# Kernel optimization log

Hardware: AMD Instinct MI355X
Metric: run time of the kernel (lower is better)

Reference implementation:

```python
import jax, jax.numpy as jnp
import numpy as np

HID, BOT, C, HEADS, K, SCALES, HZN = 32, 8, 16, 4, 3, 4, 12


def layer_norm(x, g, b, eps=1e-5):
    m = jnp.mean(x, axis=-1, keepdims=True)
    v = jnp.var(x, axis=-1, keepdims=True)
    return (x - m) * jax.lax.rsqrt(v + eps) * g + b


def setup_inputs() -> dict:
    B, T, N = 8, 32, 1500
    keys = iter(jax.random.split(jax.random.key(0), 64))
    def nrm(shape, s=0.05):
        return jax.random.normal(next(keys), shape, jnp.float32) * s
    x = jax.random.normal(next(keys), (B, T, N), jnp.float32)
    adj = (jax.random.uniform(next(keys), (N, N)) < 0.01).astype(jnp.float32)
    return dict(
        x=x, adj=adj,
        dw_w=nrm((1, 1, K)), dw_b=jnp.zeros((1,)),
        bn1_g=jnp.ones((1,)), bn1_b=jnp.zeros((1,)),
        pw_w=nrm((C, 1)), pw_b=jnp.zeros((C,)),
        bn2_g=jnp.ones((C,)), bn2_b=jnp.zeros((C,)),
        feat_w=nrm((C, HID)), feat_b=jnp.zeros((HID,)),
        scale_w=nrm((SCALES, HID, HID)), scale_b=jnp.zeros((SCALES, HID)),
        scale_ln_g=jnp.ones((SCALES, HID)), scale_ln_b=jnp.zeros((SCALES, HID)),
        fusion_weight=jnp.exp(-0.5 * jnp.arange(SCALES, dtype=jnp.float32)),
        fus_lo_w=nrm((HID, BOT)), fus_lo_b=jnp.zeros((BOT,)),
        fus_hi_w=nrm((BOT, HID)), fus_hi_b=jnp.zeros((HID,)),
        sp_ln_g=jnp.ones((HID,)), sp_ln_b=jnp.zeros((HID,)),
        qkv_lo_w=nrm((HID, 3 * BOT)), qkv_lo_b=jnp.zeros((3 * BOT,)),
        qkv_hi_w=nrm((3 * BOT, 3 * HID)), qkv_hi_b=jnp.zeros((3 * HID,)),
        graph_U=nrm((N, BOT)), graph_V=nrm((BOT, N)),
        adj_mix=jnp.array(0.0, jnp.float32), adj_scale=jnp.array(1.0, jnp.float32),
        out_lo_w=nrm((HID, BOT)), out_lo_b=jnp.zeros((BOT,)),
        out_hi_w=nrm((BOT, HID)), out_hi_b=jnp.zeros((HID,)),
        at_ln_g=jnp.ones((HID,)), at_ln_b=jnp.zeros((HID,)),
        pred_lo_w=nrm((HID, BOT)), pred_lo_b=jnp.zeros((BOT,)),
        mid_ln_g=jnp.ones((BOT,)), mid_ln_b=jnp.zeros((BOT,)),
        pred_hi_w=nrm((BOT, HZN)), pred_hi_b=jnp.zeros((HZN,)),
        log_decay=jnp.array(-2.3, jnp.float32),
        gate_w1=nrm((HID, BOT)), gate_b1=jnp.zeros((BOT,)),
        gate_w2=nrm((BOT, HZN)), gate_b2=jnp.zeros((HZN,)),
    )


def reference(x, adj, dw_w, dw_b, bn1_g, bn1_b, pw_w, pw_b, bn2_g, bn2_b,
              feat_w, feat_b, scale_w, scale_b, scale_ln_g, scale_ln_b,
              fusion_weight, fus_lo_w, fus_lo_b, fus_hi_w, fus_hi_b,
              sp_ln_g, sp_ln_b, qkv_lo_w, qkv_lo_b, qkv_hi_w, qkv_hi_b,
              graph_U, graph_V, adj_mix, adj_scale,
              out_lo_w, out_lo_b, out_hi_w, out_hi_b, at_ln_g, at_ln_b,
              pred_lo_w, pred_lo_b, mid_ln_g, mid_ln_b, pred_hi_w, pred_hi_b,
              log_decay, gate_w1, gate_b1, gate_w2, gate_b2):
    B, T, N = x.shape
    # ---- temporal feature extraction: depthwise-separable conv, eval-mode BN ----
    s = x.transpose(0, 2, 1).reshape(B * N, 1, T)  # per-node series [B*N,1,T]
    dw = jax.lax.conv_general_dilated(
        s, dw_w, (1,), 'SAME', dimension_numbers=('NCH', 'OIH', 'NCH'))
    dw = jax.nn.relu((dw + dw_b[None, :, None]) * bn1_g[None, :, None] + bn1_b[None, :, None])
    pw = jnp.einsum('bit,oi->bot', dw, pw_w) + pw_b[None, :, None]  # pointwise 1x1
    pw = jax.nn.relu(pw * bn2_g[None, :, None] + bn2_b[None, :, None])
    h = pw.mean(-1).reshape(B, N, C) @ feat_w + feat_b  # [B,N,HID]
    # ---- multi-scale spatial diffusion over adjacency powers ----
    eye = jnp.eye(N, dtype=x.dtype)
    a_hat = adj + eye
    a_hat = a_hat / (jnp.sum(a_hat, axis=-1, keepdims=True) + 1e-8)
    a2 = a_hat @ a_hat
    hops = [eye, a_hat, a2, a2 @ a_hat]
    feats = []
    for i in range(SCALES):  # fixed, small loop over scales
        agg = h if i == 0 else jnp.einsum('nm,bmh->bnh', hops[i], h)
        t = agg @ scale_w[i] + scale_b[i]
        feats.append(jax.nn.relu(layer_norm(t, scale_ln_g[i], scale_ln_b[i])))
    alpha = jax.nn.softmax(fusion_weight)
    fused = sum(alpha[i] * feats[i] for i in range(SCALES))
    out = (fused @ fus_lo_w + fus_lo_b) @ fus_hi_w + fus_hi_b  # bottleneck fusion
    h = layer_norm(out + h, sp_ln_g, sp_ln_b)
    # ---- low-rank adaptive graph attention ----
    qkv = (h @ qkv_lo_w + qkv_lo_b) @ qkv_hi_w + qkv_hi_b  # [B,N,3*HID]
    q, k, v = jnp.split(qkv, 3, axis=-1)
    hd = HID // HEADS
    to_heads = lambda t: t.reshape(B, N, HEADS, hd).transpose(0, 2, 1, 3)
    q, k, v = to_heads(q), to_heads(k), to_heads(v)
    scores = jnp.einsum('bhnd,bhmd->bhnm', q, k) / jnp.sqrt(jnp.float32(hd))
    struct = graph_U @ graph_V + jax.nn.sigmoid(adj_mix) * adj_scale * adj  # [N,N]
    attn = jax.nn.softmax(scores + struct[None, None], axis=-1)
    o = jnp.einsum('bhnm,bhmd->bhnd', attn, v).transpose(0, 2, 1, 3).reshape(B, N, HID)
    o = (o @ out_lo_w + out_lo_b) @ out_hi_w + out_hi_b
    h = layer_norm(o + h, at_ln_g, at_ln_b)
    # ---- gated horizon predictor with learned exponential decay ----
    x_mid = jax.nn.relu(layer_norm(h @ pred_lo_w + pred_lo_b, mid_ln_g, mid_ln_b))
    init_pred = x_mid @ pred_hi_w + pred_hi_b  # [B,N,HZN]
    gate = jax.nn.sigmoid(jax.nn.relu(h @ gate_w1 + gate_b1) @ gate_w2 + gate_b2)
    tdec = jnp.arange(1, HZN + 1, dtype=x.dtype)  # [HZN]
    prog = x[:, -1, :, None] * jnp.exp(-jnp.exp(log_decay) * tdec)
    return gate * init_pred + (1.0 - gate) * prog
```

## Files before the change

### kernel.cpp

```cpp
#include <hip/hip_runtime.h>
#include <math.h>

#define NN 1500
#define BB 8
#define TT 32
#define HIDD 32
#define BOTT 8
#define CC 16
#define NHEADS 4
#define NSCALES 4
#define HZNN 12
#define BC (BB*HIDD)
#define CAP 128
#define MC 128
#define PROWS 1536
#define KS_STRIDE 24
#define VS_STRIDE 136

typedef _Float16 f16;
typedef __attribute__((ext_vector_type(4))) _Float16 half4;
typedef __attribute__((ext_vector_type(4))) float floatx4;

__global__ void k_prep_temporal(const float* __restrict__ adj,
                                const float* __restrict__ gV,
                                int* __restrict__ sidx, float* __restrict__ sval,
                                float* __restrict__ sraw, int* __restrict__ scnt,
                                float* __restrict__ VgT,
                                f16* __restrict__ Qh, f16* __restrict__ Kh,
                                f16* __restrict__ VT,
                                const float* __restrict__ x,
    const float* __restrict__ dw_w, const float* __restrict__ dw_b,
    const float* __restrict__ bn1_g, const float* __restrict__ bn1_b,
    const float* __restrict__ pw_w, const float* __restrict__ pw_b,
    const float* __restrict__ bn2_g, const float* __restrict__ bn2_b,
    const float* __restrict__ feat_w, const float* __restrict__ feat_b,
    float* __restrict__ h0) {
  if (blockIdx.x < NN) {
    int n = blockIdx.x;
    int tid = threadIdx.x;
    const float* row = adj + (size_t)n * NN;
    __shared__ int cnt;
    __shared__ float red[4];
    __shared__ float s_inv;
    float ssum = 0.f;
    for (int m = tid; m < NN; m += 256) ssum += row[m];
    for (int off = 32; off > 0; off >>= 1) ssum += __shfl_down(ssum, off, 64);
    if ((tid & 63) == 0) red[tid >> 6] = ssum;
    if (tid == 0) cnt = 0;
    __syncthreads();
    if (tid == 0) {
      float tot = red[0] + red[1] + red[2] + red[3] + 1.0f;
      s_inv = 1.0f / (tot + 1e-8f);
    }
    __syncthreads();
    float inv = s_inv;
    for (int m = tid; m < NN; m += 256) {
      float a = row[m];
      if (a != 0.f || m == n) {
        int pos = atomicAdd(&cnt, 1);
        if (pos < CAP) {
          sidx[n * CAP + pos] = m;
          sval[n * CAP + pos] = (a + (m == n ? 1.f : 0.f)) * inv;
          sraw[n * CAP + pos] = a;
        }
      }
    }
    __syncthreads();
    if (tid == 0) scnt[n] = min(cnt, CAP);
    if (n == 0) {
      for (int m = tid; m < NN; m += 256) {
#pragma unroll
        for (int j = 0; j < 8; ++j) VgT[m * 8 + j] = gV[j * NN + m];
      }
    }
    if (n == 2) {
      for (int idx = tid; idx < 32 * 36 * 16; idx += 256) {
        int bb = idx / (36 * 16), rem = idx % (36 * 16);
        size_t off = ((size_t)bb * PROWS + NN + rem / 16) * 16 + (rem % 16);
        Qh[off] = (f16)0.f;
        Kh[off] = (f16)0.f;
      }
      for (int idx = tid; idx < 32 * PROWS; idx += 256) {
        int bb = idx / PROWS, m = idx % PROWS;
        VT[((size_t)bb * 16 + 8) * PROWS + m] = (f16)((m < NN) ? 1.f : 0.f);
      }
      for (int idx = tid; idx < 32 * 8 * 36; idx += 256) {
        int bb = idx / (8 * 36), rem = idx % (8 * 36);
        VT[((size_t)bb * 16 + rem / 36) * PROWS + NN + (rem % 36)] = (f16)0.f;
      }
    }
  } else {
    int tid = (blockIdx.x - NN) * 256 + threadIdx.x;
    if (tid >= BB * NN) return;
    int b = tid / NN, n = tid % NN;
    float s[TT];
#pragma unroll
    for (int t = 0; t < TT; ++t) s[t] = x[(size_t)b * TT * NN + (size_t)t * NN + n];
    float w0 = dw_w[0], w1 = dw_w[1], w2 = dw_w[2];
    float db = dw_b[0], g1v = bn1_g[0], b1v = bn1_b[0];
    float dwr[TT];
#pragma unroll
    for (int t = 0; t < TT; ++t) {
      float left  = (t > 0)      ? s[t - 1] : 0.f;
      float right = (t < TT - 1) ? s[t + 1] : 0.f;
      float v = left * w0 + s[t] * w1 + right * w2;
      v = (v + db) * g1v + b1v;
      dwr[t] = fmaxf(v, 0.f);
    }
    float mo[CC];
#pragma unroll
    for (int o = 0; o < CC; ++o) mo[o] = 0.f;
    for (int t = 0; t < TT; ++t) {
      float d = dwr[t];
#pragma unroll
      for (int o = 0; o < CC; ++o) {
        float v = (d * pw_w[o] + pw_b[o]) * bn2_g[o] + bn2_b[o];
        mo[o] += fmaxf(v, 0.f);
      }
    }
#pragma unroll
    for (int o = 0; o < CC; ++o) mo[o] *= (1.f / TT);
    float* dst = h0 + (size_t)n * BC + b * HIDD;
    for (int j = 0; j < HIDD; ++j) {
      float acc = feat_b[j];
#pragma unroll
      for (int o = 0; o < CC; ++o) acc += mo[o] * feat_w[o * HIDD + j];
      dst[j] = acc;
    }
  }
}

__global__ void k_spmm_sp(const int* __restrict__ sidx, const float* __restrict__ sval,
                          const int* __restrict__ scnt,
                          const float* __restrict__ X, float* __restrict__ Y) {
  int n = blockIdx.x;
  int tid = threadIdx.x;
  __shared__ int   li[CAP];
  __shared__ float lv[CAP];
  int cnt = scnt[n];
  if (tid < cnt) { li[tid] = sidx[n * CAP + tid]; lv[tid] = sval[n * CAP + tid]; }
  __syncthreads();
  float acc = 0.f;
  for (int e = 0; e < cnt; ++e) acc += lv[e] * X[(size_t)li[e] * BC + tid];
  Y[(size_t)n * BC + tid] = acc;
}

__global__ void k_fuse_qkv(
    const float* __restrict__ h0, const float* __restrict__ g1,
    const float* __restrict__ g2, const float* __restrict__ g3,
    const float* __restrict__ scale_w, const float* __restrict__ scale_b,
    const float* __restrict__ sln_g, const float* __restrict__ sln_b,
    const float* __restrict__ fusion_w,
    const float* __restrict__ fus_lo_w, const float* __restrict__ fus_lo_b,
    const float* __restrict__ fus_hi_w, const float* __restrict__ fus_hi_b,
    const float* __restrict__ sp_g, const float* __restrict__ sp_b,
    const float* __restrict__ qkv_lo_w, const float* __restrict__ qkv_lo_b,
    const float* __restrict__ qkv_hi_w, const float* __restrict__ qkv_hi_b,
    const float* __restrict__ gU, const float* __restrict__ VgT,
    float* __restrict__ h_out,
    float* __restrict__ Qw, float* __restrict__ Kw, float* __restrict__ Vw,
    f16* __restrict__ Qh, f16* __restrict__ Kh, f16* __restrict__ VT) {
  int tid = threadIdx.x;
  int gr = tid >> 4, l = tid & 15;
  int row = blockIdx.x * 16 + gr;
  int b = row / NN, n = row % NN;
  size_t rofs = (size_t)n * BC + b * HIDD;
  int j0 = 2 * l;
  float fw0 = fusion_w[0], fw1 = fusion_w[1], fw2 = fusion_w[2], fw3 = fusion_w[3];
  float fm = fmaxf(fmaxf(fw0, fw1), fmaxf(fw2, fw3));
  float e0 = __expf(fw0 - fm), e1 = __expf(fw1 - fm), e2 = __expf(fw2 - fm), e3 = __expf(fw3 - fm);
  float einv = 1.f / (e0 + e1 + e2 + e3);
  float alpha[4] = {e0 * einv, e1 * einv, e2 * einv, e3 * einv};
  const float* srcp[4] = {h0, g1, g2, g3};
  float fused[2] = {0.f, 0.f};
#pragma unroll
  for (int i = 0; i < NSCALES; ++i) {
    const float* sp = srcp[i] + rofs;
    float src[32];
#pragma unroll
    for (int k4 = 0; k4 < 8; ++k4) {
      float4 f = *(const float4*)(sp + k4 * 4);
      src[k4 * 4] = f.x; src[k4 * 4 + 1] = f.y; src[k4 * 4 + 2] = f.z; src[k4 * 4 + 3] = f.w;
    }
    const float* W = scale_w + i * HIDD * HIDD;
    float t0 = scale_b[i * HIDD + j0], t1v = scale_b[i * HIDD + j0 + 1];
#pragma unroll
    for (int k = 0; k < 32; ++k) {
      float2 w = *(const float2*)(W + k * HIDD + j0);
      t0 += src[k] * w.x; t1v += src[k] * w.y;
    }
    float s1 = t0 + t1v;
    float s2 = t0 * t0 + t1v * t1v;
    s1 += __shfl_xor(s1, 1, 16); s1 += __shfl_xor(s1, 2, 16);
    s1 += __shfl_xor(s1, 4, 16); s1 += __shfl_xor(s1, 8, 16);
    s2 += __shfl_xor(s2, 1, 16); s2 += __shfl_xor(s2, 2, 16);
    s2 += __shfl_xor(s2, 4, 16); s2 += __shfl_xor(s2, 8, 16);
    float mean = s1 * (1.f / 32.f);
    float var = s2 * (1.f / 32.f) - mean * mean;
    float r = rsqrtf(var + 1e-5f);
    float a = alpha[i];
    float tn0 = (t0 - mean) * r * sln_g[i * HIDD + j0] + sln_b[i * HIDD + j0];
    float tn1 = (t1v - mean) * r * sln_g[i * HIDD + j0 + 1] + sln_b[i * HIDD + j0 + 1];
    fused[0] += a * fmaxf(tn0, 0.f);
    fused[1] += a * fmaxf(tn1, 0.f);
  }
  float lo[BOTT];
#pragma unroll
  for (int o = 0; o < BOTT; ++o) {
    float acc = fused[0] * fus_lo_w[j0 * BOTT + o] + fused[1] * fus_lo_w[(j0 + 1) * BOTT + o];
    acc += __shfl_xor(acc, 1, 16); acc += __shfl_xor(acc, 2, 16);
    acc += __shfl_xor(acc, 4, 16); acc += __shfl_xor(acc, 8, 16);
    lo[o] = acc + fus_lo_b[o];
  }
  float2 hv2 = *(const float2*)(h0 + rofs + j0);
  float pre[2] = {hv2.x, hv2.y};
#pragma unroll
  for (int jj = 0; jj < 2; ++jj) {
    float acc = fus_hi_b[j0 + jj] + pre[jj];
#pragma unroll
    for (int o = 0; o < BOTT; ++o) acc += lo[o] * fus_hi_w[o * HIDD + j0 + jj];
    pre[jj] = acc;
  }
  {
    float s1 = pre[0] + pre[1];
    float s2 = pre[0] * pre[0] + pre[1] * pre[1];
    s1 += __shfl_xor(s1, 1, 16); s1 += __shfl_xor(s1, 2, 16);
    s1 += __shfl_xor(s1, 4, 16); s1 += __shfl_xor(s1, 8, 16);
    s2 += __shfl_xor(s2, 1, 16); s2 += __shfl_xor(s2, 2, 16);
    s2 += __shfl_xor(s2, 4, 16); s2 += __shfl_xor(s2, 8, 16);
    float mean = s1 * (1.f / 32.f);
    float var = s2 * (1.f / 32.f) - mean * mean;
    float r = rsqrtf(var + 1e-5f);
#pragma unroll
    for (int jj = 0; jj < 2; ++jj)
      pre[jj] = (pre[jj] - mean) * r * sp_g[j0 + jj] + sp_b[j0 + jj];
  }
  *(float2*)(h_out + (size_t)row * HIDD + j0) = make_float2(pre[0], pre[1]);
  float t1[24];
#pragma unroll
  for (int o = 0; o < 24; ++o) {
    float acc = pre[0] * qkv_lo_w[j0 * 24 + o] + pre[1] * qkv_lo_w[(j0 + 1) * 24 + o];
    acc += __shfl_xor(acc, 1, 16); acc += __shfl_xor(acc, 2, 16);
    acc += __shfl_xor(acc, 4, 16); acc += __shfl_xor(acc, 8, 16);
    t1[o] = acc + qkv_lo_b[o];
  }
  const float scl = 0.35355339059327373f;
  int sub = l >> 3, d = l & 7;
#pragma unroll
  for (int part = 0; part < 3; ++part) {
    float* dst = (part == 0) ? Qw : (part == 1) ? Kw : Vw;
#pragma unroll
    for (int hh = 0; hh < 2; ++hh) {
      int hd = sub * 2 + hh;
      int p = part * 32 + hd * 8 + d;
      float acc = qkv_hi_b[p];
#pragma unroll
      for (int o = 0; o < 24; ++o) acc += t1[o] * qkv_hi_w[o * 96 + p];
      dst[(((size_t)b * NHEADS + hd) * NN + n) * 8 + d] = acc;
      int bh = b * NHEADS + hd;
      if (part == 0) {
        Qh[((size_t)bh * PROWS + n) * 16 + d] = (f16)(acc * scl);
        Qh[((size_t)bh * PROWS + n) * 16 + 8 + d] = (f16)gU[n * 8 + d];
      } else if (part == 1) {
        Kh[((size_t)bh * PROWS + n) * 16 + d] = (f16)acc;
        Kh[((size_t)bh * PROWS + n) * 16 + 8 + d] = (f16)VgT[n * 8 + d];
      } else {
        VT[((size_t)bh * 16 + d) * PROWS + n] = (f16)acc;
      }
    }
  }
}

__global__ void __launch_bounds__(256, 4)
k_attn_mfma(const f16* __restrict__ Qh, const f16* __restrict__ Kh,
            const f16* __restrict__ VT, float* __restrict__ P) {
  int bh = blockIdx.x;
  int tile = blockIdx.y;
  int tid = threadIdx.x;
  int wave = tid >> 6, lane = tid & 63;
  int quad = lane >> 4, l16 = lane & 15;
  __shared__ f16 Ks[MC * KS_STRIDE];
  __shared__ f16 Vs[16 * VS_STRIDE];
  int n0 = tile * 64 + wave * 16;
  half4 qf = *(const half4*)(Qh + ((size_t)bh * PROWS + n0 + l16) * 16 + quad * 4);
  floatx4 acc = {0.f, 0.f, 0.f, 0.f};
  for (int m0 = 0; m0 < PROWS; m0 += MC) {
    __syncthreads();
    {
      int row = tid >> 1, h = (tid & 1) * 8;
      *(float4*)(Ks + row * KS_STRIDE + h) =
          *(const float4*)(Kh + ((size_t)bh * PROWS + m0 + row) * 16 + h);
      int d = tid >> 4, c = (tid & 15) * 8;
      *(float4*)(Vs + d * VS_STRIDE + c) =
          *(const float4*)(VT + ((size_t)bh * 16 + d) * PROWS + m0 + c);
    }
    __syncthreads();
#pragma unroll
    for (int mt = 0; mt < MC / 16; ++mt) {
      half4 kf = *(const half4*)(Ks + (mt * 16 + l16) * KS_STRIDE + quad * 4);
      floatx4 s = __builtin_amdgcn_mfma_f32_16x16x16f16(
          kf, qf, (floatx4){0.f, 0.f, 0.f, 0.f}, 0, 0, 0);
      half4 pf;
      pf[0] = (f16)__expf(s[0]);
      pf[1] = (f16)__expf(s[1]);
      pf[2] = (f16)__expf(s[2]);
      pf[3] = (f16)__expf(s[3]);
      half4 vf = *(const half4*)(Vs + l16 * VS_STRIDE + mt * 16 + quad * 4);
      acc = __builtin_amdgcn_mfma_f32_16x16x16f16(pf, vf, acc, 0, 0, 0);
    }
  }
  if (l16 < 9) {
#pragma unroll
    for (int r = 0; r < 4; ++r) {
      int n = n0 + quad * 4 + r;
      P[((size_t)bh * PROWS + n) * 12 + l16] = acc[r];
    }
  }
}

__global__ void k_attn_sp(const float* __restrict__ Qw, const float* __restrict__ Kw,
                          const float* __restrict__ Vw,
                          const float* __restrict__ gU, const float* __restrict__ VgT,
                          const int* __restrict__ sidx, const float* __restrict__ sraw,
                          const int* __restrict__ scnt,
                          const float* __restrict__ adj_mix, const float* __restrict__ adj_scale,
                          float* __restrict__ P) {
  int bh = blockIdx.x;
  int tid = threadIdx.x;
  int g = tid >> 3, p = tid & 7;
  float smix = adj_scale[0] / (1.f + __expf(-adj_mix[0]));
  const float scl = 0.35355339059327373f;
  const float* Kb = Kw + (size_t)bh * NN * 8;
  const float* Vb = Vw + (size_t)bh * NN * 8;
  for (int rr = 0; rr < 4; ++rr) {
    int n = blockIdx.y * 128 + g * 4 + rr;
    float acc[8] = {0.f, 0.f, 0.f, 0.f, 0.f, 0.f, 0.f, 0.f};
    float sm = 0.f;
    if (n < NN) {
      const float* qp = Qw + ((size_t)bh * NN + n) * 8;
      const float* up = gU + n * 8;
      float qv[16];
#pragma unroll
      for (int d = 0; d < 8; ++d) { qv[d] = qp[d] * scl; qv[8 + d] = up[d]; }
      int cnt = scnt[n];
      for (int e = p; e < cnt; e += 8) {
        int m = sidx[n * CAP + e];
        float a = sraw[n * CAP + e];
        if (a != 0.f) {
          const float* kp = Kb + (size_t)m * 8;
          float4 k0 = *(const float4*)(kp);
          float4 k1 = *(const float4*)(kp + 4);
          const float* gp = VgT + (size_t)m * 8;
          float4 k2 = *(const float4*)(gp);
          float4 k3 = *(const float4*)(gp + 4);
          float s = qv[0]*k0.x + qv[1]*k0.y + qv[2]*k0.z + qv[3]*k0.w
                  + qv[4]*k1.x + qv[5]*k1.y + qv[6]*k1.z + qv[7]*k1.w
                  + qv[8]*k2.x + qv[9]*k2.y + qv[10]*k2.z + qv[11]*k2.w
                  + qv[12]*k3.x + qv[13]*k3.y + qv[14]*k3.z + qv[15]*k3.w;
          float ep = __expf(s);
          float dlt = ep * (__expf(smix * a) - 1.f);
          sm += dlt;
          const float* vp = Vb + (size_t)m * 8;
          float4 v0 = *(const float4*)(vp);
          float4 v1 = *(const float4*)(vp + 4);
          acc[0] += dlt * v0.x; acc[1] += dlt * v0.y; acc[2] += dlt * v0.z; acc[3] += dlt * v0.w;
          acc[4] += dlt * v1.x; acc[5] += dlt * v1.y; acc[6] += dlt * v1.z; acc[7] += dlt * v1.w;
        }
      }
    }
    sm += __shfl_xor(sm, 1, 8); sm += __shfl_xor(sm, 2, 8); sm += __shfl_xor(sm, 4, 8);
#pragma unroll
    for (int d = 0; d < 8; ++d) {
      acc[d] += __shfl_xor(acc[d], 1, 8);
      acc[d] += __shfl_xor(acc[d], 2, 8);
      acc[d] += __shfl_xor(acc[d], 4, 8);
    }
    float val = acc[0];
#pragma unroll
    for (int d = 1; d < 8; ++d) if (p == d) val = acc[d];
    if (n < NN) {
      float* dst = P + ((size_t)(32 + bh) * PROWS + n) * 12;
      dst[p] = val;
      if (p == 0) dst[8] = sm;
    }
  }
}

__global__ void k_final(const float* __restrict__ P, const float* __restrict__ h_in,
    const float* __restrict__ x,
    const float* __restrict__ out_lo_w, const float* __restrict__ out_lo_b,
    const float* __restrict__ out_hi_w, const float* __restrict__ out_hi_b,
    const float* __restrict__ at_g, const float* __restrict__ at_b,
    const float* __restrict__ pred_lo_w, const float* __restrict__ pred_lo_b,
    const float* __restrict__ mid_g, const float* __restrict__ mid_b,
    const float* __restrict__ pred_hi_w, const float* __restrict__ pred_hi_b,
    const float* __restrict__ log_decay,
    const float* __restrict__ gate_w1, const float* __restrict__ gate_b1,
    const float* __restrict__ gate_w2, const float* __restrict__ gate_b2,
    float* __restrict__ out) {
  int tid = threadIdx.x;
  int gr = tid >> 3, l = tid & 7;
  int row = blockIdx.x * 32 + gr;
  int b = row / NN, n = row % NN;
  int j0 = 4 * l;
  int hd = l >> 1, d0 = (l & 1) * 4;
  int bh = b * NHEADS + hd;
  float av[4] = {0.f, 0.f, 0.f, 0.f};
  float smt = 0.f;
#pragma unroll
  for (int z = 0; z < 2; ++z) {
    const float* q = P + ((size_t)(z * 32 + bh) * PROWS + n) * 12;
    float4 a4 = *(const float4*)(q + d0);
    av[0] += a4.x; av[1] += a4.y; av[2] += a4.z; av[3] += a4.w;
    smt += q[8];
  }
  float oinv = 1.f / smt;
  float ov4[4];
#pragma unroll
  for (int d = 0; d < 4; ++d) ov4[d] = av[d] * oinv;
  float lo[BOTT];
#pragma unroll
  for (int o = 0; o < BOTT; ++o) {
    float acc = 0.f;
#pragma unroll
    for (int jj = 0; jj < 4; ++jj) acc += ov4[jj] * out_lo_w[(j0 + jj) * BOTT + o];
    acc += __shfl_xor(acc, 1, 8); acc += __shfl_xor(acc, 2, 8); acc += __shfl_xor(acc, 4, 8);
    lo[o] = acc + out_lo_b[o];
  }
  float4 hin4 = *(const float4*)(h_in + (size_t)row * HIDD + j0);
  float pre[4] = {hin4.x, hin4.y, hin4.z, hin4.w};
#pragma unroll
  for (int jj = 0; jj < 4; ++jj) {
    float acc = out_hi_b[j0 + jj] + pre[jj];
#pragma unroll
    for (int o = 0; o < BOTT; ++o) acc += lo[o] * out_hi_w[o * HIDD + j0 + jj];
    pre[jj] = acc;
  }
  float h2[4];
  {
    float s1 = pre[0] + pre[1] + pre[2] + pre[3];
    float s2 = pre[0]*pre[0] + pre[1]*pre[1] + pre[2]*pre[2] + pre[3]*pre[3];
    s1 += __shfl_xor(s1, 1, 8); s1 += __shfl_xor(s1, 2, 8); s1 += __shfl_xor(s1, 4, 8);
    s2 += __shfl_xor(s2, 1, 8); s2 += __shfl_xor(s2, 2, 8); s2 += __shfl_xor(s2, 4, 8);
    float mean = s1 * (1.f / 32.f);
    float var = s2 * (1.f / 32.f) - mean * mean;
    float r = rsqrtf(var + 1e-5f);
#pragma unroll
    for (int jj = 0; jj < 4; ++jj)
      h2[jj] = (pre[jj] - mean) * r * at_g[j0 + jj] + at_b[j0 + jj];
  }
  float pl[BOTT];
#pragma unroll
  for (int o = 0; o < BOTT; ++o) {
    float acc = 0.f;
#pragma unroll
    for (int jj = 0; jj < 4; ++jj) acc += h2[jj] * pred_lo_w[(j0 + jj) * BOTT + o];
    acc += __shfl_xor(acc, 1, 8); acc += __shfl_xor(acc, 2, 8); acc += __shfl_xor(acc, 4, 8);
    pl[o] = acc + pred_lo_b[o];
  }
  float xm[BOTT];
  {
    float m = 0.f;
#pragma unroll
    for (int o = 0; o < BOTT; ++o) m += pl[o];
    m *= (1.f / BOTT);
    float var = 0.f;
#pragma unroll
    for (int o = 0; o < BOTT; ++o) { float d = pl[o] - m; var += d * d; }
    var *= (1.f / BOTT);
    float r = rsqrtf(var + 1e-5f);
#pragma unroll
    for (int o = 0; o < BOTT; ++o)
      xm[o] = fmaxf((pl[o] - m) * r * mid_g[o] + mid_b[o], 0.f);
  }
  float ga[BOTT];
#pragma unroll
  for (int o = 0; o < BOTT; ++o) {
    float acc = 0.f;
#pragma unroll
    for (int jj = 0; jj < 4; ++jj) acc += h2[jj] * gate_w1[(j0 + jj) * BOTT + o];
    acc += __shfl_xor(acc, 1, 8); acc += __shfl_xor(acc, 2, 8); acc += __shfl_xor(acc, 4, 8);
    ga[o] = fmaxf(acc + gate_b1[o], 0.f);
  }
  float xl = x[(size_t)b * TT * NN + (size_t)(TT - 1) * NN + n];
  float dec = __expf(log_decay[0]);
#pragma unroll
  for (int ii = 0; ii < 2; ++ii) {
    int i = l + ii * 8;
    if (i < HZNN) {
      float accp = pred_hi_b[i];
#pragma unroll
      for (int o = 0; o < BOTT; ++o) accp += xm[o] * pred_hi_w[o * HZNN + i];
      float accg = gate_b2[i];
#pragma unroll
      for (int o = 0; o < BOTT; ++o) accg += ga[o] * gate_w2[o * HZNN + i];
      float gt = 1.f / (1.f + __expf(-accg));
      float pr = xl * __expf(-dec * (float)(i + 1));
      out[(size_t)row * HZNN + i] = gt * accp + (1.f - gt) * pr;
    }
  }
}

extern "C" void kernel_launch(void* const* d_in, const int* in_sizes, int n_in,
                              void* d_out, int out_size, void* d_ws, size_t ws_size,
                              hipStream_t stream) {
  const float* x          = (const float*)d_in[0];
  const float* adj        = (const float*)d_in[1];
  const float* dw_w       = (const float*)d_in[2];
  const float* dw_b       = (const float*)d_in[3];
  const float* bn1_g      = (const float*)d_in[4];
  const float* bn1_b      = (const float*)d_in[5];
  const float* pw_w       = (const float*)d_in[6];
  const float* pw_b       = (const float*)d_in[7];
  const float* bn2_g      = (const float*)d_in[8];
  const float* bn2_b      = (const float*)d_in[9];
  const float* feat_w     = (const float*)d_in[10];
  const float* feat_b     = (const float*)d_in[11];
  const float* scale_w    = (const float*)d_in[12];
  const float* scale_b    = (const float*)d_in[13];
  const float* scale_ln_g = (const float*)d_in[14];
  const float* scale_ln_b = (const float*)d_in[15];
  const float* fusion_w   = (const float*)d_in[16];
  const float* fus_lo_w   = (const float*)d_in[17];
  const float* fus_lo_b   = (const float*)d_in[18];
  const float* fus_hi_w   = (const float*)d_in[19];
  const float* fus_hi_b   = (const float*)d_in[20];
  const float* sp_ln_g    = (const float*)d_in[21];
  const float* sp_ln_b    = (const float*)d_in[22];
  const float* qkv_lo_w   = (const float*)d_in[23];
  const float* qkv_lo_b   = (const float*)d_in[24];
  const float* qkv_hi_w   = (const float*)d_in[25];
  const float* qkv_hi_b   = (const float*)d_in[26];
  const float* graph_U    = (const float*)d_in[27];
  const float* graph_V    = (const float*)d_in[28];
  const float* adj_mix    = (const float*)d_in[29];
  const float* adj_scale  = (const float*)d_in[30];
  const float* out_lo_w   = (const float*)d_in[31];
  const float* out_lo_b   = (const float*)d_in[32];
  const float* out_hi_w   = (const float*)d_in[33];
  const float* out_hi_b   = (const float*)d_in[34];
  const float* at_ln_g    = (const float*)d_in[35];
  const float* at_ln_b    = (const float*)d_in[36];
  const float* pred_lo_w  = (const float*)d_in[37];
  const float* pred_lo_b  = (const float*)d_in[38];
  const float* mid_ln_g   = (const float*)d_in[39];
  const float* mid_ln_b   = (const float*)d_in[40];
  const float* pred_hi_w  = (const float*)d_in[41];
  const float* pred_hi_b  = (const float*)d_in[42];
  const float* log_decay  = (const float*)d_in[43];
  const float* gate_w1    = (const float*)d_in[44];
  const float* gate_b1    = (const float*)d_in[45];
  const float* gate_w2    = (const float*)d_in[46];
  const float* gate_b2    = (const float*)d_in[47];

  float* ws = (float*)d_ws;
  float* h0    = ws;
  float* g1    = h0 + (size_t)NN * BC;
  float* g2    = g1 + (size_t)NN * BC;
  float* g3    = g2 + (size_t)NN * BC;
  float* hfull = g3 + (size_t)NN * BC;
  float* Qw    = hfull + (size_t)BB * NN * HIDD;
  float* Kw    = Qw + (size_t)BB * NN * HIDD;
  float* Vw    = Kw + (size_t)BB * NN * HIDD;
  float* VgT   = Vw + (size_t)BB * NN * HIDD;
  float* sval  = VgT + (size_t)NN * 8;
  float* sraw  = sval + (size_t)NN * CAP;
  int*   sidx  = (int*)(sraw + (size_t)NN * CAP);
  int*   scnt  = sidx + (size_t)NN * CAP;
  float* P     = (float*)(scnt + NN + 3);
  P = (float*)(((uintptr_t)P + 15) & ~(uintptr_t)15);
  f16* Qh = (f16*)(P + (size_t)2 * 32 * PROWS * 12);
  f16* Kh = Qh + (size_t)32 * PROWS * 16;
  f16* VT = Kh + (size_t)32 * PROWS * 16;

  k_prep_temporal<<<NN + 47, 256, 0, stream>>>(
      adj, graph_V, sidx, sval, sraw, scnt, VgT, Qh, Kh, VT,
      x, dw_w, dw_b, bn1_g, bn1_b, pw_w, pw_b, bn2_g, bn2_b, feat_w, feat_b, h0);
  k_spmm_sp<<<NN, 256, 0, stream>>>(sidx, sval, scnt, h0, g1);
  k_spmm_sp<<<NN, 256, 0, stream>>>(sidx, sval, scnt, g1, g2);
  k_spmm_sp<<<NN, 256, 0, stream>>>(sidx, sval, scnt, g2, g3);
  k_fuse_qkv<<<(BB * NN) / 16, 256, 0, stream>>>(
      h0, g1, g2, g3, scale_w, scale_b, scale_ln_g, scale_ln_b, fusion_w,
      fus_lo_w, fus_lo_b, fus_hi_w, fus_hi_b, sp_ln_g, sp_ln_b,
      qkv_lo_w, qkv_lo_b, qkv_hi_w, qkv_hi_b, graph_U, VgT,
      hfull, Qw, Kw, Vw, Qh, Kh, VT);
  k_attn_mfma<<<dim3(32, PROWS / 64), 256, 0, stream>>>(Qh, Kh, VT, P);
  k_attn_sp<<<dim3(32, 12), 256, 0, stream>>>(
      Qw, Kw, Vw, graph_U, VgT, sidx, sraw, scnt, adj_mix, adj_scale, P);
  k_final<<<(BB * NN) / 32, 256, 0, stream>>>(
      P, hfull, x, out_lo_w, out_lo_b, out_hi_w, out_hi_b, at_ln_g, at_ln_b,
      pred_lo_w, pred_lo_b, mid_ln_g, mid_ln_b, pred_hi_w, pred_hi_b,
      log_decay, gate_w1, gate_b1, gate_w2, gate_b2, (float*)d_out);
}
```

Baseline: 255.6 us.

## Merge sparse-correction attention into MFMA attention kernel and drop fp32 QKV copies

The dense MFMA attention and the sparse adjacency-correction pass now run as one launch, with the sparse pass as extra blockIdx.y tiles. The sparse pass reads the f16 Qh/Kh/VT buffers instead of separate fp32 Q/K/V copies, so k_fuse_qkv no longer writes those copies. The spmm kernel also reads neighbour indices and weights straight from global memory instead of staging them in LDS behind a barrier. This cuts one launch and some global writes, but the sparse correction loses precision by using f16 inputs. Its loads also become strided (VT is transposed) and may coalesce less well.

```diff
diff --git a/kernel.cpp b/kernel.cpp
--- a/kernel.cpp
+++ b/kernel.cpp
@@ -135,13 +135,11 @@
                           const float* __restrict__ X, float* __restrict__ Y) {
   int n = blockIdx.x;
   int tid = threadIdx.x;
-  __shared__ int   li[CAP];
-  __shared__ float lv[CAP];
   int cnt = scnt[n];
-  if (tid < cnt) { li[tid] = sidx[n * CAP + tid]; lv[tid] = sval[n * CAP + tid]; }
-  __syncthreads();
+  const int* ip = sidx + n * CAP;
+  const float* vp = sval + n * CAP;
   float acc = 0.f;
-  for (int e = 0; e < cnt; ++e) acc += lv[e] * X[(size_t)li[e] * BC + tid];
+  for (int e = 0; e < cnt; ++e) acc += vp[e] * X[(size_t)ip[e] * BC + tid];
   Y[(size_t)n * BC + tid] = acc;
 }
 
@@ -158,7 +156,6 @@
     const float* __restrict__ qkv_hi_w, const float* __restrict__ qkv_hi_b,
     const float* __restrict__ gU, const float* __restrict__ VgT,
     float* __restrict__ h_out,
-    float* __restrict__ Qw, float* __restrict__ Kw, float* __restrict__ Vw,
     f16* __restrict__ Qh, f16* __restrict__ Kh, f16* __restrict__ VT) {
   int tid = threadIdx.x;
   int gr = tid >> 4, l = tid & 15;
@@ -248,7 +245,6 @@
   int sub = l >> 3, d = l & 7;
 #pragma unroll
   for (int part = 0; part < 3; ++part) {
-    float* dst = (part == 0) ? Qw : (part == 1) ? Kw : Vw;
 #pragma unroll
     for (int hh = 0; hh < 2; ++hh) {
       int hd = sub * 2 + hh;
@@ -256,7 +252,6 @@
       float acc = qkv_hi_b[p];
 #pragma unroll
       for (int o = 0; o < 24; ++o) acc += t1[o] * qkv_hi_w[o * 96 + p];
-      dst[(((size_t)b * NHEADS + hd) * NN + n) * 8 + d] = acc;
       int bh = b * NHEADS + hd;
       if (part == 0) {
         Qh[((size_t)bh * PROWS + n) * 16 + d] = (f16)(acc * scl);
@@ -272,116 +267,101 @@
 }
 
 __global__ void __launch_bounds__(256, 4)
-k_attn_mfma(const f16* __restrict__ Qh, const f16* __restrict__ Kh,
-            const f16* __restrict__ VT, float* __restrict__ P) {
+k_attn(const f16* __restrict__ Qh, const f16* __restrict__ Kh,
+       const f16* __restrict__ VT,
+       const int* __restrict__ sidx, const float* __restrict__ sraw,
+       const int* __restrict__ scnt,
+       const float* __restrict__ adj_mix, const float* __restrict__ adj_scale,
+       float* __restrict__ P) {
   int bh = blockIdx.x;
-  int tile = blockIdx.y;
   int tid = threadIdx.x;
-  int wave = tid >> 6, lane = tid & 63;
-  int quad = lane >> 4, l16 = lane & 15;
   __shared__ f16 Ks[MC * KS_STRIDE];
   __shared__ f16 Vs[16 * VS_STRIDE];
-  int n0 = tile * 64 + wave * 16;
-  half4 qf = *(const half4*)(Qh + ((size_t)bh * PROWS + n0 + l16) * 16 + quad * 4);
-  floatx4 acc = {0.f, 0.f, 0.f, 0.f};
-  for (int m0 = 0; m0 < PROWS; m0 += MC) {
-    __syncthreads();
-    {
-      int row = tid >> 1, h = (tid & 1) * 8;
-      *(float4*)(Ks + row * KS_STRIDE + h) =
-          *(const float4*)(Kh + ((size_t)bh * PROWS + m0 + row) * 16 + h);
-      int d = tid >> 4, c = (tid & 15) * 8;
-      *(float4*)(Vs + d * VS_STRIDE + c) =
-          *(const float4*)(VT + ((size_t)bh * 16 + d) * PROWS + m0 + c);
-    }
-    __syncthreads();
-#pragma unroll
-    for (int mt = 0; mt < MC / 16; ++mt) {
-      half4 kf = *(const half4*)(Ks + (mt * 16 + l16) * KS_STRIDE + quad * 4);
-      floatx4 s = __builtin_amdgcn_mfma_f32_16x16x16f16(
-          kf, qf, (floatx4){0.f, 0.f, 0.f, 0.f}, 0, 0, 0);
-      half4 pf;
-      pf[0] = (f16)__expf(s[0]);
-      pf[1] = (f16)__expf(s[1]);
-      pf[2] = (f16)__expf(s[2]);
-      pf[3] = (f16)__expf(s[3]);
-      half4 vf = *(const half4*)(Vs + l16 * VS_STRIDE + mt * 16 + quad * 4);
-      acc = __builtin_amdgcn_mfma_f32_16x16x16f16(pf, vf, acc, 0, 0, 0);
-    }
-  }
-  if (l16 < 9) {
-#pragma unroll
-    for (int r = 0; r < 4; ++r) {
-      int n = n0 + quad * 4 + r;
-      P[((size_t)bh * PROWS + n) * 12 + l16] = acc[r];
-    }
-  }
-}
-
-__global__ void k_attn_sp(const float* __restrict__ Qw, const float* __restrict__ Kw,
-                          const float* __restrict__ Vw,
-                          const float* __restrict__ gU, const float* __restrict__ VgT,
-                          const int* __restrict__ sidx, const float* __restrict__ sraw,
-                          const int* __restrict__ scnt,
-                          const float* __restrict__ adj_mix, const float* __restrict__ adj_scale,
-                          float* __restrict__ P) {
-  int bh = blockIdx.x;
-  int tid = threadIdx.x;
-  int g = tid >> 3, p = tid & 7;
-  float smix = adj_scale[0] / (1.f + __expf(-adj_mix[0]));
-  const float scl = 0.35355339059327373f;
-  const float* Kb = Kw + (size_t)bh * NN * 8;
-  const float* Vb = Vw + (size_t)bh * NN * 8;
-  for (int rr = 0; rr < 4; ++rr) {
-    int n = blockIdx.y * 128 + g * 4 + rr;
-    float acc[8] = {0.f, 0.f, 0.f, 0.f, 0.f, 0.f, 0.f, 0.f};
-    float sm = 0.f;
-    if (n < NN) {
-      const float* qp = Qw + ((size_t)bh * NN + n) * 8;
-      const float* up = gU + n * 8;
-      float qv[16];
-#pragma unroll
-      for (int d = 0; d < 8; ++d) { qv[d] = qp[d] * scl; qv[8 + d] = up[d]; }
-      int cnt = scnt[n];
-      for (int e = p; e < cnt; e += 8) {
-        int m = sidx[n * CAP + e];
-        float a = sraw[n * CAP + e];
-        if (a != 0.f) {
-          const float* kp = Kb + (size_t)m * 8;
-          float4 k0 = *(const float4*)(kp);
-          float4 k1 = *(const float4*)(kp + 4);
-          const float* gp = VgT + (size_t)m * 8;
-          float4 k2 = *(const float4*)(gp);
-          float4 k3 = *(const float4*)(gp + 4);
-          float s = qv[0]*k0.x + qv[1]*k0.y + qv[2]*k0.z + qv[3]*k0.w
-                  + qv[4]*k1.x + qv[5]*k1.y + qv[6]*k1.z + qv[7]*k1.w
-                  + qv[8]*k2.x + qv[9]*k2.y + qv[10]*k2.z + qv[11]*k2.w
-                  + qv[12]*k3.x + qv[13]*k3.y + qv[14]*k3.z + qv[15]*k3.w;
-          float ep = __expf(s);
-          float dlt = ep * (__expf(smix * a) - 1.f);
-          sm += dlt;
-          const float* vp = Vb + (size_t)m * 8;
-          float4 v0 = *(const float4*)(vp);
-          float4 v1 = *(const float4*)(vp + 4);
-          acc[0] += dlt * v0.x; acc[1] += dlt * v0.y; acc[2] += dlt * v0.z; acc[3] += dlt * v0.w;
-          acc[4] += dlt * v1.x; acc[5] += dlt * v1.y; acc[6] += dlt * v1.z; acc[7] += dlt * v1.w;
+  if (blockIdx.y < 24) {
+    int tile = blockIdx.y;
+    int wave = tid >> 6, lane = tid & 63;
+    int quad = lane >> 4, l16 = lane & 15;
+    int n0 = tile * 64 + wave * 16;
+    half4 qf = *(const half4*)(Qh + ((size_t)bh * PROWS + n0 + l16) * 16 + quad * 4);
+    floatx4 acc = {0.f, 0.f, 0.f, 0.f};
+    for (int m0 = 0; m0 < PROWS; m0 += MC) {
+      __syncthreads();
+      {
+        int row = tid >> 1, h = (tid & 1) * 8;
+        *(float4*)(Ks + row * KS_STRIDE + h) =
+            *(const float4*)(Kh + ((size_t)bh * PROWS + m0 + row) * 16 + h);
+        int d = tid >> 4, c = (tid & 15) * 8;
+        *(float4*)(Vs + d * VS_STRIDE + c) =
+            *(const float4*)(VT + ((size_t)bh * 16 + d) * PROWS + m0 + c);
+      }
+      __syncthreads();
+#pragma unroll
+      for (int mt = 0; mt < MC / 16; ++mt) {
+        half4 kf = *(const half4*)(Ks + (mt * 16 + l16) * KS_STRIDE + quad * 4);
+        floatx4 s = __builtin_amdgcn_mfma_f32_16x16x16f16(
+            kf, qf, (floatx4){0.f, 0.f, 0.f, 0.f}, 0, 0, 0);
+        half4 pf;
+        pf[0] = (f16)__expf(s[0]);
+        pf[1] = (f16)__expf(s[1]);
+        pf[2] = (f16)__expf(s[2]);
+        pf[3] = (f16)__expf(s[3]);
+        half4 vf = *(const half4*)(Vs + l16 * VS_STRIDE + mt * 16 + quad * 4);
+        acc = __builtin_amdgcn_mfma_f32_16x16x16f16(pf, vf, acc, 0, 0, 0);
+      }
+    }
+    if (l16 < 9) {
+#pragma unroll
+      for (int r = 0; r < 4; ++r) {
+        int n = n0 + quad * 4 + r;
+        P[((size_t)bh * PROWS + n) * 12 + l16] = acc[r];
+      }
+    }
+  } else {
+    int ytile = blockIdx.y - 24;
+    int g = tid >> 3, p = tid & 7;
+    float smix = adj_scale[0] / (1.f + __expf(-adj_mix[0]));
+    for (int rr = 0; rr < 4; ++rr) {
+      int n = ytile * 128 + g * 4 + rr;
+      float acc[8] = {0.f, 0.f, 0.f, 0.f, 0.f, 0.f, 0.f, 0.f};
+      float sm = 0.f;
+      if (n < NN) {
+        const f16* qp = Qh + ((size_t)bh * PROWS + n) * 16;
+        float qv[16];
+#pragma unroll
+        for (int d = 0; d < 16; ++d) qv[d] = (float)qp[d];
+        int cnt = scnt[n];
+        for (int e = p; e < cnt; e += 8) {
+          int m = sidx[n * CAP + e];
+          float a = sraw[n * CAP + e];
+          if (a != 0.f) {
+            const f16* kp = Kh + ((size_t)bh * PROWS + m) * 16;
+            float s = 0.f;
+#pragma unroll
+            for (int d = 0; d < 16; ++d) s += qv[d] * (float)kp[d];
+            float ep = __expf(s);
+            float dlt = ep * (__expf(smix * a) - 1.f);
+            sm += dlt;
+#pragma unroll
+            for (int d = 0; d < 8; ++d)
+              acc[d] += dlt * (float)VT[((size_t)bh * 16 + d) * PROWS + m];
+          }
         }
       }
-    }
-    sm += __shfl_xor(sm, 1, 8); sm += __shfl_xor(sm, 2, 8); sm += __shfl_xor(sm, 4, 8);
-#pragma unroll
-    for (int d = 0; d < 8; ++d) {
-      acc[d] += __shfl_xor(acc[d], 1, 8);
-      acc[d] += __shfl_xor(acc[d], 2, 8);
-      acc[d] += __shfl_xor(acc[d], 4, 8);
-    }
-    float val = acc[0];
-#pragma unroll
-    for (int d = 1; d < 8; ++d) if (p == d) val = acc[d];
-    if (n < NN) {
-      float* dst = P + ((size_t)(32 + bh) * PROWS + n) * 12;
-      dst[p] = val;
-      if (p == 0) dst[8] = sm;
+      sm += __shfl_xor(sm, 1, 8); sm += __shfl_xor(sm, 2, 8); sm += __shfl_xor(sm, 4, 8);
+#pragma unroll
+      for (int d = 0; d < 8; ++d) {
+        acc[d] += __shfl_xor(acc[d], 1, 8);
+        acc[d] += __shfl_xor(acc[d], 2, 8);
+        acc[d] += __shfl_xor(acc[d], 4, 8);
+      }
+      float val = acc[0];
+#pragma unroll
+      for (int d = 1; d < 8; ++d) if (p == d) val = acc[d];
+      if (n < NN) {
+        float* dst = P + ((size_t)(32 + bh) * PROWS + n) * 12;
+        dst[p] = val;
+        if (p == 0) dst[8] = sm;
+      }
     }
   }
 }
@@ -559,10 +539,7 @@
   float* g2    = g1 + (size_t)NN * BC;
   float* g3    = g2 + (size_t)NN * BC;
   float* hfull = g3 + (size_t)NN * BC;
-  float* Qw    = hfull + (size_t)BB * NN * HIDD;
-  float* Kw    = Qw + (size_t)BB * NN * HIDD;
-  float* Vw    = Kw + (size_t)BB * NN * HIDD;
-  float* VgT   = Vw + (size_t)BB * NN * HIDD;
+  float* VgT   = hfull + (size_t)BB * NN * HIDD;
   float* sval  = VgT + (size_t)NN * 8;
   float* sraw  = sval + (size_t)NN * CAP;
   int*   sidx  = (int*)(sraw + (size_t)NN * CAP);
@@ -583,10 +560,9 @@
       h0, g1, g2, g3, scale_w, scale_b, scale_ln_g, scale_ln_b, fusion_w,
       fus_lo_w, fus_lo_b, fus_hi_w, fus_hi_b, sp_ln_g, sp_ln_b,
       qkv_lo_w, qkv_lo_b, qkv_hi_w, qkv_hi_b, graph_U, VgT,
-      hfull, Qw, Kw, Vw, Qh, Kh, VT);
-  k_attn_mfma<<<dim3(32, PROWS / 64), 256, 0, stream>>>(Qh, Kh, VT, P);
-  k_attn_sp<<<dim3(32, 12), 256, 0, stream>>>(
-      Qw, Kw, Vw, graph_U, VgT, sidx, sraw, scnt, adj_mix, adj_scale, P);
+      hfull, Qh, Kh, VT);
+  k_attn<<<dim3(32, 36), 256, 0, stream>>>(
+      Qh, Kh, VT, sidx, sraw, scnt, adj_mix, adj_scale, P);
   k_final<<<(BB * NN) / 32, 256, 0, stream>>>(
       P, hfull, x, out_lo_w, out_lo_b, out_hi_w, out_hi_b, at_ln_g, at_ln_b,
       pred_lo_w, pred_lo_b, mid_ln_g, mid_ln_b, pred_hi_w, pred_hi_b,
```

Result: no change. 255.0 us (-0.2%).
